# Kernel tuning notes

Measured on AMD Instinct MI355X. Metric: run time of the kernel, lower is better.

Reference implementation:

```python
import jax, jax.numpy as jnp
from jax import lax
import numpy as np

CH = 16      # channel_n
HID = 128    # update MLP width


def setup_inputs() -> dict:
    key = jax.random.key(0)
    ks = jax.random.split(key, 7)
    B, H, W = 4, 224, 224
    x = jax.random.uniform(ks[0], (B, CH, H, W), dtype=jnp.float32)
    # perception: Conv2d(16 -> 48, 3x3, pad 1, no bias), OIHW
    w_percep = jax.random.normal(ks[1], (CH * 3, CH, 3, 3), jnp.float32) * 0.05
    # update MLP: 1x1 convs == pointwise linears over channels
    w1 = jax.random.normal(ks[2], (HID, CH * 3), jnp.float32) * 0.05
    b1 = jax.random.normal(ks[3], (HID,), jnp.float32) * 0.01
    w2 = jax.random.normal(ks[4], (HID, HID), jnp.float32) * 0.05
    b2 = jax.random.normal(ks[5], (HID,), jnp.float32) * 0.01
    w3 = jax.random.normal(ks[6], (CH, HID), jnp.float32) * 0.05  # no bias
    return {"x": x, "w_percep": w_percep, "w1": w1, "b1": b1,
            "w2": w2, "b2": b2, "w3": w3, "steps": 40}


def reference(x, w_percep, w1, b1, w2, b2, w3, steps):
    dn = ("NCHW", "OIHW", "NCHW")

    def step(x, _):
        # 3x3 perception conv, same padding  -> [B, 48, H, W]
        p = lax.conv_general_dilated(x, w_percep, (1, 1), "SAME",
                                     dimension_numbers=dn)
        # pointwise conv-MLP (1x1 convs as channel einsums)
        h = jax.nn.relu(jnp.einsum("bchw,oc->bohw", p, w1) + b1[None, :, None, None])
        h = jax.nn.relu(jnp.einsum("bchw,oc->bohw", h, w2) + b2[None, :, None, None])
        dx = jnp.einsum("bchw,oc->bohw", h, w3)
        # residual update + clamp to [0, 1] (eval mode: no fire mask)
        return jnp.clip(x + dx, 0.0, 1.0), None

    x, _ = lax.scan(step, x, None, length=steps)
    return x
```

## Files before the change

### kernel.cpp

```cpp
#include <hip/hip_runtime.h>


typedef __attribute__((ext_vector_type(8))) short short8;
typedef __attribute__((ext_vector_type(4))) float float4v;
typedef __attribute__((ext_vector_type(2))) unsigned int uint2v;

#define MFMA16(a, b, c) __builtin_amdgcn_mfma_f32_16x16x32_bf16((a), (b), (c), 0, 0, 0)

__device__ __forceinline__ short f2bf(float f) {
  unsigned u = __builtin_bit_cast(unsigned, f);
  return (short)((u + 0x8000u) >> 16);
}

__device__ __forceinline__ unsigned pk2bf(float a, float b) {
#if __has_builtin(__builtin_amdgcn_cvt_pk_bf16_f32)
  typedef __attribute__((ext_vector_type(2))) __bf16 bf2;
  bf2 r = __builtin_amdgcn_cvt_pk_bf16_f32(a, b);
  return __builtin_bit_cast(unsigned, r);
#else
  unsigned ua = __builtin_bit_cast(unsigned, a), ub = __builtin_bit_cast(unsigned, b);
  return ((ua + 0x8000u) >> 16) | (((ub + 0x8000u) >> 16) << 16);
#endif
}

__device__ __forceinline__ void async16(const void* g, void* l) {
  __builtin_amdgcn_global_load_lds((const __attribute__((address_space(1))) void*)g,
                                   (__attribute__((address_space(3))) void*)l,
                                   16, 0, 0);
}

__device__ __forceinline__ void sync_lds() {
  asm volatile("s_waitcnt lgkmcnt(0)\n\ts_barrier" ::: "memory");
}

#define WS_WE    0
#define WS_W2    43008
#define WS_W3    77824
#define WS_B1    82944
#define WS_B2    83456
#define WS_X32A  83968
#define WS_X32B  12929024
#define WS_X16A  25774080
#define WS_X16B  32196608

__global__ void prep_x(const float* __restrict__ x, float* __restrict__ x32,
                       short* __restrict__ x16) {
  int i = blockIdx.x * 256 + threadIdx.x;
  int w = i % 224;
  int h = (i / 224) % 224;
  int c = (i / 50176) & 15;
  int bb = i / 802816;
  float v = x[i];
  int o = ((bb * 224 + h) * 224 + w) * 16 + c;
  x32[o] = v;
  x16[o] = f2bf(v);
}

__global__ void prep_w(const float* __restrict__ wp, const float* __restrict__ w1,
                       const float* __restrict__ b1, const float* __restrict__ w2,
                       const float* __restrict__ b2, const float* __restrict__ w3,
                       short* __restrict__ wE, short* __restrict__ w2t,
                       short* __restrict__ w3t, float* __restrict__ b1p,
                       float* __restrict__ b2p) {
  int i = blockIdx.x * 256 + threadIdx.x;
  if (i < 21504) {
    int o = i / 168, k = i % 168;
    float v = 0.f;
    if (k < 144) {
      int off = k >> 4, c = k & 15;
      for (int c3 = 0; c3 < 48; ++c3)
        v += w1[o * 48 + c3] * wp[c3 * 144 + c * 9 + off];
    }
    wE[i] = f2bf(v);
  } else if (i < 38912) {
    int j = i - 21504;
    int n = j / 136, kk = j % 136;
    w2t[j] = (kk < 128) ? f2bf(w2[n * 128 + kk]) : (short)0;
  } else if (i < 41472) {
    int j = i - 38912;
    float v = 0.f;
    if (j < 2176) {
      int n = j / 136, kk = j % 136;
      if (kk < 128) v = w3[n * 128 + kk];
    }
    w3t[j] = f2bf(v);
  } else if (i < 41600) {
    int p = i - 41472;
    b1p[p] = b1[p];
  } else {
    int p = i - 41600;
    b2p[p] = b2[p];
  }
}

template <bool LAST>
__global__ __launch_bounds__(512, 4) void ca_step(
    const short* __restrict__ wEg, const short* __restrict__ w2g,
    const short* __restrict__ w3g, const float* __restrict__ b1p,
    const float* __restrict__ b2p, const float* __restrict__ xs32,
    const short* __restrict__ xs16, float* __restrict__ xd32,
    short* __restrict__ xd16, float* __restrict__ dout) {
  __shared__ short sXH[4 * 3616];
  __shared__ short sBUF[2 * 2 * 2176];
  __shared__ short sH2[2 * 2 * 2176];

  const int tid = threadIdx.x;
  const int lane = tid & 63;
  const int wv = tid >> 6;
  const int c16 = lane & 15;
  const int q = lane >> 4;
  const int q8 = q * 8;
  const int qh = q >> 1;
  const int c0 = (q & 1) * 8;

  const int blk = blockIdx.x;
  const int b = blk / 112;
  const int h0 = (blk % 112) * 2;

  const short8 z8 = {0, 0, 0, 0, 0, 0, 0, 0};
  for (int t = wv; t < 28; t += 8) {
    int hr = t / 7, ck = t % 7;
    int hh = h0 - 1 + hr;
    char* l = (char*)sXH + hr * 7232 + 32 + ck * 1024;
    if (hh >= 0 && hh < 224) {
      const char* g = (const char*)xs16 + ((size_t)(b * 224 + hh) * 224) * 32 + ck * 1024;
      async16(g + lane * 16, l);
    } else {
      *(short8*)(l + lane * 16) = z8;
    }
  }
  if (tid < 16) {
    int hr = tid >> 2, wch = tid & 3;
    int colb = (wch < 2) ? 0 : 225;
    *(short8*)((char*)sXH + hr * 7232 + colb * 32 + (wch & 1) * 16) = z8;
  }

  if (wv < 4) {
    const int wq = wv;
    const int obase = 32 * wq;
    short8 wf[5][2];
#pragma unroll
    for (int kc = 0; kc < 5; ++kc)
#pragma unroll
      for (int n = 0; n < 2; ++n)
        wf[kc][n] = *(const short8*)(wEg + (obase + 16 * n + c16) * 168 + kc * 32 + q8);
    float4v bH[2];
#pragma unroll
    for (int n = 0; n < 2; ++n)
      bH[n] = *(const float4v*)(b1p + obase + 16 * n + 4 * q);

    __syncthreads();

    for (int j = 0; j < 16; ++j) {
      if (j < 14) {
        const int t0 = 2 * j, t1 = t0 + 1;
        const int hb0 = ((t0 / 14) * 226 + (t0 % 14) * 16) * 16;
        const int hb1 = ((t1 / 14) * 226 + (t1 % 14) * 16) * 16;
        float4v acc[2][2];
#pragma unroll
        for (int tt = 0; tt < 2; ++tt)
#pragma unroll
          for (int n = 0; n < 2; ++n) acc[tt][n] = (float4v){0.f, 0.f, 0.f, 0.f};
        __builtin_amdgcn_s_setprio(1);
#pragma unroll
        for (int kc = 0; kc < 5; ++kc) {
          int off = kc * 2 + qh;
          if (off > 8) off = 8;
          int dy = (off * 11) >> 5;
          int dxx = off - dy * 3;
          const int ao = (dy * 226 + dxx + c16) * 16 + c0;
          short8 a0 = *(const short8*)(sXH + hb0 + ao);
          short8 a1 = *(const short8*)(sXH + hb1 + ao);
#pragma unroll
          for (int n = 0; n < 2; ++n) {
            acc[0][n] = MFMA16(wf[kc][n], a0, acc[0][n]);
            acc[1][n] = MFMA16(wf[kc][n], a1, acc[1][n]);
          }
        }
        __builtin_amdgcn_s_setprio(0);
#pragma unroll
        for (int tt = 0; tt < 2; ++tt) {
          short* dst = sBUF + ((j & 1) * 2 + tt) * 2176 + c16 * 136;
#pragma unroll
          for (int n = 0; n < 2; ++n) {
            unsigned d0 = pk2bf(fmaxf(acc[tt][n][0] + bH[n][0], 0.f),
                                fmaxf(acc[tt][n][1] + bH[n][1], 0.f));
            unsigned d1 = pk2bf(fmaxf(acc[tt][n][2] + bH[n][2], 0.f),
                                fmaxf(acc[tt][n][3] + bH[n][3], 0.f));
            *(uint2v*)(dst + obase + 16 * n + 4 * q) = (uint2v){d0, d1};
          }
        }
      }
      sync_lds();
    }
  } else {
    const int g = wv - 4;
    const int obase = 32 * g;
    short8 w2f[4][2];
    short8 w3f[4];
#pragma unroll
    for (int kc = 0; kc < 4; ++kc)
#pragma unroll
      for (int n = 0; n < 2; ++n)
        w2f[kc][n] = *(const short8*)(w2g + (obase + 16 * n + c16) * 136 + kc * 32 + q8);
#pragma unroll
    for (int kc = 0; kc < 4; ++kc)
      w3f[kc] = *(const short8*)(w3g + c16 * 136 + kc * 32 + q8);
    float4v bG[2];
#pragma unroll
    for (int n = 0; n < 2; ++n)
      bG[n] = *(const float4v*)(b2p + obase + 16 * n + 4 * q);

    __syncthreads();

    for (int j = 0; j < 16; ++j) {
      float4v acc3;
      int cb3 = 0, hglob3 = 0;
      const bool doG3 = (g < 2) && (j >= 2);
      if (doG3) {
        const int t3 = 2 * (j - 2) + g;
        cb3 = (t3 % 14) * 16; hglob3 = h0 + t3 / 14;
        const size_t pix = (size_t)(b * 224 + hglob3) * 224 + cb3 + c16;
        acc3 = *(const float4v*)(xs32 + pix * 16 + q * 4);
      }
      if (j >= 1 && j <= 14) {
        const short* srcA = sBUF + (((j - 1) & 1) * 2 + 0) * 2176;
        const short* srcB = sBUF + (((j - 1) & 1) * 2 + 1) * 2176;
        float4v acc2[2][2];
#pragma unroll
        for (int tt = 0; tt < 2; ++tt)
#pragma unroll
          for (int n = 0; n < 2; ++n) acc2[tt][n] = (float4v){0.f, 0.f, 0.f, 0.f};
        __builtin_amdgcn_s_setprio(1);
#pragma unroll
        for (int kc = 0; kc < 4; ++kc) {
          short8 aA = *(const short8*)(srcA + c16 * 136 + kc * 32 + q8);
          short8 aB = *(const short8*)(srcB + c16 * 136 + kc * 32 + q8);
#pragma unroll
          for (int n = 0; n < 2; ++n) {
            acc2[0][n] = MFMA16(w2f[kc][n], aA, acc2[0][n]);
            acc2[1][n] = MFMA16(w2f[kc][n], aB, acc2[1][n]);
          }
        }
        __builtin_amdgcn_s_setprio(0);
#pragma unroll
        for (int tt = 0; tt < 2; ++tt) {
          short* dsth2 = sH2 + ((j & 1) * 2 + tt) * 2176 + c16 * 136;
#pragma unroll
          for (int n = 0; n < 2; ++n) {
            unsigned d0 = pk2bf(fmaxf(acc2[tt][n][0] + bG[n][0], 0.f),
                                fmaxf(acc2[tt][n][1] + bG[n][1], 0.f));
            unsigned d1 = pk2bf(fmaxf(acc2[tt][n][2] + bG[n][2], 0.f),
                                fmaxf(acc2[tt][n][3] + bG[n][3], 0.f));
            *(uint2v*)(dsth2 + obase + 16 * n + 4 * q) = (uint2v){d0, d1};
          }
        }
      }
      if (doG3) {
        const short* srch2 = sH2 + (((j - 1) & 1) * 2 + g) * 2176;
        __builtin_amdgcn_s_setprio(1);
#pragma unroll
        for (int kc = 0; kc < 4; ++kc) {
          short8 a = *(const short8*)(srch2 + c16 * 136 + kc * 32 + q8);
          acc3 = MFMA16(w3f[kc], a, acc3);
        }
        __builtin_amdgcn_s_setprio(0);
        float4v vv;
#pragma unroll
        for (int r = 0; r < 4; ++r) vv[r] = fminf(fmaxf(acc3[r], 0.f), 1.f);
        if (LAST) {
#pragma unroll
          for (int r = 0; r < 4; ++r)
            dout[((size_t)(b * 16 + q * 4 + r) * 224 + hglob3) * 224 + cb3 + c16] = vv[r];
        } else {
          const size_t pix = (size_t)(b * 224 + hglob3) * 224 + cb3 + c16;
          *(float4v*)(xd32 + pix * 16 + q * 4) = vv;
          *(uint2v*)(xd16 + pix * 16 + q * 4) =
              (uint2v){pk2bf(vv[0], vv[1]), pk2bf(vv[2], vv[3])};
        }
      }
      sync_lds();
    }
  }
}

extern "C" void kernel_launch(void* const* d_in, const int* in_sizes, int n_in,
                              void* d_out, int out_size, void* d_ws, size_t ws_size,
                              hipStream_t stream) {
  const float* x  = (const float*)d_in[0];
  const float* wp = (const float*)d_in[1];
  const float* w1 = (const float*)d_in[2];
  const float* b1 = (const float*)d_in[3];
  const float* w2 = (const float*)d_in[4];
  const float* b2 = (const float*)d_in[5];
  const float* w3 = (const float*)d_in[6];

  char* ws = (char*)d_ws;
  short* wEg = (short*)(ws + WS_WE);
  short* w2g = (short*)(ws + WS_W2);
  short* w3g = (short*)(ws + WS_W3);
  float* b1p = (float*)(ws + WS_B1);
  float* b2p = (float*)(ws + WS_B2);
  float* X32[2] = {(float*)(ws + WS_X32A), (float*)(ws + WS_X32B)};
  short* X16[2] = {(short*)(ws + WS_X16A), (short*)(ws + WS_X16B)};

  prep_x<<<12544, 256, 0, stream>>>(x, X32[0], X16[0]);
  prep_w<<<163, 256, 0, stream>>>(wp, w1, b1, w2, b2, w3, wEg, w2g, w3g, b1p, b2p);

  for (int s = 0; s < 39; ++s) {
    int sb = s & 1;
    ca_step<false><<<448, 512, 0, stream>>>(wEg, w2g, w3g, b1p, b2p,
                                            X32[sb], X16[sb],
                                            X32[1 - sb], X16[1 - sb], nullptr);
  }
  ca_step<true><<<448, 512, 0, stream>>>(wEg, w2g, w3g, b1p, b2p,
                                         X32[1], X16[1],
                                         X32[0], X16[0], (float*)d_out);
}
```

Baseline: 985.7 us.

## Replace per-iteration block barriers with LDS flag counters between producer/consumer waves

Removes the lockstep s_barrier at each pipeline iteration and replaces it with per-buffer LDS counters that producer waves atomically bump and consumer waves spin on with s_sleep. Stage-1, stage-2 and stage-3 waves can then run ahead of one another within the double-buffer limits instead of waiting for the slowest stage every iteration. The cost is spin-polling traffic on LDS and atomics, and a risk of ordering or visibility bugs because the flag targets are hand-derived.

Result: slower. 1.268 ms (+28.6%).

```diff
diff --git a/kernel.cpp b/kernel.cpp
--- a/kernel.cpp
+++ b/kernel.cpp
@@ -29,8 +29,15 @@
                                    16, 0, 0);
 }
 
-__device__ __forceinline__ void sync_lds() {
-  asm volatile("s_waitcnt lgkmcnt(0)\n\ts_barrier" ::: "memory");
+__device__ __forceinline__ void wait_flag(const volatile unsigned* f, unsigned target) {
+  while (*f < target) __builtin_amdgcn_s_sleep(1);
+  __builtin_amdgcn_sched_barrier(0);
+  asm volatile("" ::: "memory");
+}
+
+__device__ __forceinline__ void bump_flag(unsigned* f, int lane) {
+  asm volatile("s_waitcnt lgkmcnt(0)" ::: "memory");
+  if (lane == 0) atomicAdd(f, 1u);
 }
 
 #define WS_WE    0
@@ -103,6 +110,7 @@
   __shared__ short sXH[4 * 3616];
   __shared__ short sBUF[2 * 2 * 2176];
   __shared__ short sH2[2 * 2 * 2176];
+  __shared__ unsigned sFLAG[8];
 
   const int tid = threadIdx.x;
   const int lane = tid & 63;
@@ -116,6 +124,8 @@
   const int blk = blockIdx.x;
   const int b = blk / 112;
   const int h0 = (blk % 112) * 2;
+
+  if (tid < 8) sFLAG[tid] = 0;
 
   const short8 z8 = {0, 0, 0, 0, 0, 0, 0, 0};
   for (int t = wv; t < 28; t += 8) {
@@ -151,47 +161,46 @@
 
     __syncthreads();
 
-    for (int j = 0; j < 16; ++j) {
-      if (j < 14) {
-        const int t0 = 2 * j, t1 = t0 + 1;
-        const int hb0 = ((t0 / 14) * 226 + (t0 % 14) * 16) * 16;
-        const int hb1 = ((t1 / 14) * 226 + (t1 % 14) * 16) * 16;
-        float4v acc[2][2];
-#pragma unroll
-        for (int tt = 0; tt < 2; ++tt)
-#pragma unroll
-          for (int n = 0; n < 2; ++n) acc[tt][n] = (float4v){0.f, 0.f, 0.f, 0.f};
-        __builtin_amdgcn_s_setprio(1);
-#pragma unroll
-        for (int kc = 0; kc < 5; ++kc) {
-          int off = kc * 2 + qh;
-          if (off > 8) off = 8;
-          int dy = (off * 11) >> 5;
-          int dxx = off - dy * 3;
-          const int ao = (dy * 226 + dxx + c16) * 16 + c0;
-          short8 a0 = *(const short8*)(sXH + hb0 + ao);
-          short8 a1 = *(const short8*)(sXH + hb1 + ao);
-#pragma unroll
-          for (int n = 0; n < 2; ++n) {
-            acc[0][n] = MFMA16(wf[kc][n], a0, acc[0][n]);
-            acc[1][n] = MFMA16(wf[kc][n], a1, acc[1][n]);
-          }
-        }
-        __builtin_amdgcn_s_setprio(0);
-#pragma unroll
-        for (int tt = 0; tt < 2; ++tt) {
-          short* dst = sBUF + ((j & 1) * 2 + tt) * 2176 + c16 * 136;
-#pragma unroll
-          for (int n = 0; n < 2; ++n) {
-            unsigned d0 = pk2bf(fmaxf(acc[tt][n][0] + bH[n][0], 0.f),
-                                fmaxf(acc[tt][n][1] + bH[n][1], 0.f));
-            unsigned d1 = pk2bf(fmaxf(acc[tt][n][2] + bH[n][2], 0.f),
-                                fmaxf(acc[tt][n][3] + bH[n][3], 0.f));
-            *(uint2v*)(dst + obase + 16 * n + 4 * q) = (uint2v){d0, d1};
-          }
-        }
-      }
-      sync_lds();
+    for (int j = 0; j < 14; ++j) {
+      const int t0 = 2 * j, t1 = t0 + 1;
+      const int hb0 = ((t0 / 14) * 226 + (t0 % 14) * 16) * 16;
+      const int hb1 = ((t1 / 14) * 226 + (t1 % 14) * 16) * 16;
+      float4v acc[2][2];
+#pragma unroll
+      for (int tt = 0; tt < 2; ++tt)
+#pragma unroll
+        for (int n = 0; n < 2; ++n) acc[tt][n] = (float4v){0.f, 0.f, 0.f, 0.f};
+      __builtin_amdgcn_s_setprio(1);
+#pragma unroll
+      for (int kc = 0; kc < 5; ++kc) {
+        int off = kc * 2 + qh;
+        if (off > 8) off = 8;
+        int dy = (off * 11) >> 5;
+        int dxx = off - dy * 3;
+        const int ao = (dy * 226 + dxx + c16) * 16 + c0;
+        short8 a0 = *(const short8*)(sXH + hb0 + ao);
+        short8 a1 = *(const short8*)(sXH + hb1 + ao);
+#pragma unroll
+        for (int n = 0; n < 2; ++n) {
+          acc[0][n] = MFMA16(wf[kc][n], a0, acc[0][n]);
+          acc[1][n] = MFMA16(wf[kc][n], a1, acc[1][n]);
+        }
+      }
+      __builtin_amdgcn_s_setprio(0);
+      if (j >= 2) wait_flag(&sFLAG[2 + (j & 1)], 4u * (unsigned)(j >> 1));
+#pragma unroll
+      for (int tt = 0; tt < 2; ++tt) {
+        short* dst = sBUF + ((j & 1) * 2 + tt) * 2176 + c16 * 136;
+#pragma unroll
+        for (int n = 0; n < 2; ++n) {
+          unsigned d0 = pk2bf(fmaxf(acc[tt][n][0] + bH[n][0], 0.f),
+                              fmaxf(acc[tt][n][1] + bH[n][1], 0.f));
+          unsigned d1 = pk2bf(fmaxf(acc[tt][n][2] + bH[n][2], 0.f),
+                              fmaxf(acc[tt][n][3] + bH[n][3], 0.f));
+          *(uint2v*)(dst + obase + 16 * n + 4 * q) = (uint2v){d0, d1};
+        }
+      }
+      bump_flag(&sFLAG[0 + (j & 1)], lane);
     }
   } else {
     const int g = wv - 4;
@@ -224,8 +233,10 @@
         acc3 = *(const float4v*)(xs32 + pix * 16 + q * 4);
       }
       if (j >= 1 && j <= 14) {
-        const short* srcA = sBUF + (((j - 1) & 1) * 2 + 0) * 2176;
-        const short* srcB = sBUF + (((j - 1) & 1) * 2 + 1) * 2176;
+        const int s1 = (j - 1) & 1;
+        wait_flag(&sFLAG[0 + s1], 4u * (unsigned)(((j - 1) >> 1) + 1));
+        const short* srcA = sBUF + (s1 * 2 + 0) * 2176;
+        const short* srcB = sBUF + (s1 * 2 + 1) * 2176;
         float4v acc2[2][2];
 #pragma unroll
         for (int tt = 0; tt < 2; ++tt)
@@ -243,6 +254,9 @@
           }
         }
         __builtin_amdgcn_s_setprio(0);
+        bump_flag(&sFLAG[2 + s1], lane);
+        if (j >= 3) wait_flag(&sFLAG[6 + (j & 1)],
+                              2u * (unsigned)((j - (2 - (j & 1))) >> 1));
 #pragma unroll
         for (int tt = 0; tt < 2; ++tt) {
           short* dsth2 = sH2 + ((j & 1) * 2 + tt) * 2176 + c16 * 136;
@@ -255,9 +269,14 @@
             *(uint2v*)(dsth2 + obase + 16 * n + 4 * q) = (uint2v){d0, d1};
           }
         }
+        bump_flag(&sFLAG[4 + (j & 1)], lane);
       }
       if (doG3) {
-        const short* srch2 = sH2 + (((j - 1) & 1) * 2 + g) * 2176;
+        const int i = j - 1;
+        const int s2 = i & 1;
+        wait_flag(&sFLAG[4 + s2],
+                  4u * (unsigned)(((i - (2 - s2)) >> 1) + 1));
+        const short* srch2 = sH2 + (s2 * 2 + g) * 2176;
         __builtin_amdgcn_s_setprio(1);
 #pragma unroll
         for (int kc = 0; kc < 4; ++kc) {
@@ -265,6 +284,7 @@
           acc3 = MFMA16(w3f[kc], a, acc3);
         }
         __builtin_amdgcn_s_setprio(0);
+        bump_flag(&sFLAG[6 + s2], lane);
         float4v vv;
 #pragma unroll
         for (int r = 0; r < 4; ++r) vv[r] = fminf(fmaxf(acc3[r], 0.f), 1.f);
@@ -279,7 +299,6 @@
               (uint2v){pk2bf(vv[0], vv[1]), pk2bf(vv[2], vv[3])};
         }
       }
-      sync_lds();
     }
   }
 }
```

## Rebalance layer-2 output columns across waves and remap block order

Applied to the files above, without the earlier changes.

Waves 4-7 previously split the 128 layer-2 outputs evenly at 32 each, while waves 4-5 also ran the layer-3 MFMA and residual update. The split is now uneven: waves 4-5 take 16 outputs each plus layer 3, and waves 6-7 take 48 each. The aim is to even out per-wave MFMA work so the critical path per pipeline step gets shorter. The block index is also permuted so consecutive hardware blocks come from strided row groups, likely to spread work across XCDs or improve cache locality. The cost is more registers on the heavy waves.

Measured after the change: 1.018 ms. +3.3%, slower.

```diff
diff --git a/kernel.cpp b/kernel.cpp
--- a/kernel.cpp
+++ b/kernel.cpp
@@ -113,7 +113,7 @@
   const int qh = q >> 1;
   const int c0 = (q & 1) * 8;
 
-  const int blk = blockIdx.x;
+  const int blk = (blockIdx.x & 7) * 56 + (blockIdx.x >> 3);
   const int b = blk / 112;
   const int h0 = (blk % 112) * 2;
 
@@ -195,28 +195,39 @@
     }
   } else {
     const int g = wv - 4;
-    const int obase = 32 * g;
-    short8 w2f[4][2];
+    const bool light = (g < 2);
+    const int ob2 = light ? (96 + 16 * g) : (48 * (g - 2));
+    short8 w2a[4];
+    short8 w2b[4][2];
     short8 w3f[4];
 #pragma unroll
     for (int kc = 0; kc < 4; ++kc)
-#pragma unroll
-      for (int n = 0; n < 2; ++n)
-        w2f[kc][n] = *(const short8*)(w2g + (obase + 16 * n + c16) * 136 + kc * 32 + q8);
-#pragma unroll
-    for (int kc = 0; kc < 4; ++kc)
-      w3f[kc] = *(const short8*)(w3g + c16 * 136 + kc * 32 + q8);
-    float4v bG[2];
-#pragma unroll
-    for (int n = 0; n < 2; ++n)
-      bG[n] = *(const float4v*)(b2p + obase + 16 * n + 4 * q);
+      w2a[kc] = *(const short8*)(w2g + (ob2 + c16) * 136 + kc * 32 + q8);
+    if (!light) {
+#pragma unroll
+      for (int kc = 0; kc < 4; ++kc)
+#pragma unroll
+        for (int nf = 0; nf < 2; ++nf)
+          w2b[kc][nf] = *(const short8*)(w2g + (ob2 + 16 * (nf + 1) + c16) * 136 + kc * 32 + q8);
+    } else {
+#pragma unroll
+      for (int kc = 0; kc < 4; ++kc)
+        w3f[kc] = *(const short8*)(w3g + c16 * 136 + kc * 32 + q8);
+    }
+    float4v bG[3];
+    bG[0] = *(const float4v*)(b2p + ob2 + 4 * q);
+    if (!light) {
+#pragma unroll
+      for (int nf = 1; nf < 3; ++nf)
+        bG[nf] = *(const float4v*)(b2p + ob2 + 16 * nf + 4 * q);
+    }
 
     __syncthreads();
 
     for (int j = 0; j < 16; ++j) {
       float4v acc3;
       int cb3 = 0, hglob3 = 0;
-      const bool doG3 = (g < 2) && (j >= 2);
+      const bool doG3 = light && (j >= 2);
       if (doG3) {
         const int t3 = 2 * (j - 2) + g;
         cb3 = (t3 % 14) * 16; hglob3 = h0 + t3 / 14;
@@ -226,33 +237,59 @@
       if (j >= 1 && j <= 14) {
         const short* srcA = sBUF + (((j - 1) & 1) * 2 + 0) * 2176;
         const short* srcB = sBUF + (((j - 1) & 1) * 2 + 1) * 2176;
-        float4v acc2[2][2];
-#pragma unroll
-        for (int tt = 0; tt < 2; ++tt)
-#pragma unroll
-          for (int n = 0; n < 2; ++n) acc2[tt][n] = (float4v){0.f, 0.f, 0.f, 0.f};
-        __builtin_amdgcn_s_setprio(1);
-#pragma unroll
-        for (int kc = 0; kc < 4; ++kc) {
-          short8 aA = *(const short8*)(srcA + c16 * 136 + kc * 32 + q8);
-          short8 aB = *(const short8*)(srcB + c16 * 136 + kc * 32 + q8);
-#pragma unroll
-          for (int n = 0; n < 2; ++n) {
-            acc2[0][n] = MFMA16(w2f[kc][n], aA, acc2[0][n]);
-            acc2[1][n] = MFMA16(w2f[kc][n], aB, acc2[1][n]);
-          }
-        }
-        __builtin_amdgcn_s_setprio(0);
-#pragma unroll
-        for (int tt = 0; tt < 2; ++tt) {
-          short* dsth2 = sH2 + ((j & 1) * 2 + tt) * 2176 + c16 * 136;
-#pragma unroll
-          for (int n = 0; n < 2; ++n) {
-            unsigned d0 = pk2bf(fmaxf(acc2[tt][n][0] + bG[n][0], 0.f),
-                                fmaxf(acc2[tt][n][1] + bG[n][1], 0.f));
-            unsigned d1 = pk2bf(fmaxf(acc2[tt][n][2] + bG[n][2], 0.f),
-                                fmaxf(acc2[tt][n][3] + bG[n][3], 0.f));
-            *(uint2v*)(dsth2 + obase + 16 * n + 4 * q) = (uint2v){d0, d1};
+        if (light) {
+          float4v a2[2];
+          a2[0] = (float4v){0.f, 0.f, 0.f, 0.f};
+          a2[1] = (float4v){0.f, 0.f, 0.f, 0.f};
+          __builtin_amdgcn_s_setprio(1);
+#pragma unroll
+          for (int kc = 0; kc < 4; ++kc) {
+            short8 aA = *(const short8*)(srcA + c16 * 136 + kc * 32 + q8);
+            short8 aB = *(const short8*)(srcB + c16 * 136 + kc * 32 + q8);
+            a2[0] = MFMA16(w2a[kc], aA, a2[0]);
+            a2[1] = MFMA16(w2a[kc], aB, a2[1]);
+          }
+          __builtin_amdgcn_s_setprio(0);
+#pragma unroll
+          for (int tt = 0; tt < 2; ++tt) {
+            short* dsth2 = sH2 + ((j & 1) * 2 + tt) * 2176 + c16 * 136;
+            unsigned d0 = pk2bf(fmaxf(a2[tt][0] + bG[0][0], 0.f),
+                                fmaxf(a2[tt][1] + bG[0][1], 0.f));
+            unsigned d1 = pk2bf(fmaxf(a2[tt][2] + bG[0][2], 0.f),
+                                fmaxf(a2[tt][3] + bG[0][3], 0.f));
+            *(uint2v*)(dsth2 + ob2 + 4 * q) = (uint2v){d0, d1};
+          }
+        } else {
+          float4v a2[2][3];
+#pragma unroll
+          for (int tt = 0; tt < 2; ++tt)
+#pragma unroll
+            for (int nf = 0; nf < 3; ++nf) a2[tt][nf] = (float4v){0.f, 0.f, 0.f, 0.f};
+          __builtin_amdgcn_s_setprio(1);
+#pragma unroll
+          for (int kc = 0; kc < 4; ++kc) {
+            short8 aA = *(const short8*)(srcA + c16 * 136 + kc * 32 + q8);
+            short8 aB = *(const short8*)(srcB + c16 * 136 + kc * 32 + q8);
+            a2[0][0] = MFMA16(w2a[kc], aA, a2[0][0]);
+            a2[1][0] = MFMA16(w2a[kc], aB, a2[1][0]);
+#pragma unroll
+            for (int nf = 0; nf < 2; ++nf) {
+              a2[0][nf + 1] = MFMA16(w2b[kc][nf], aA, a2[0][nf + 1]);
+              a2[1][nf + 1] = MFMA16(w2b[kc][nf], aB, a2[1][nf + 1]);
+            }
+          }
+          __builtin_amdgcn_s_setprio(0);
+#pragma unroll
+          for (int tt = 0; tt < 2; ++tt) {
+            short* dsth2 = sH2 + ((j & 1) * 2 + tt) * 2176 + c16 * 136;
+#pragma unroll
+            for (int nf = 0; nf < 3; ++nf) {
+              unsigned d0 = pk2bf(fmaxf(a2[tt][nf][0] + bG[nf][0], 0.f),
+                                  fmaxf(a2[tt][nf][1] + bG[nf][1], 0.f));
+              unsigned d1 = pk2bf(fmaxf(a2[tt][nf][2] + bG[nf][2], 0.f),
+                                  fmaxf(a2[tt][nf][3] + bG[nf][3], 0.f));
+              *(uint2v*)(dsth2 + ob2 + 16 * nf + 4 * q) = (uint2v){d0, d1};
+            }
           }
         }
       }
```
